# Optimization experiments

Measured on AMD Instinct MI355X. Metric: run time of the kernel, lower is better.

## Reference

```python
import jax, jax.numpy as jnp
import numpy as np

N = 20000      # nodes
E = 200000     # edges
IN = 128       # in_feat
OUT = 128      # out_feat
NB = 8         # num_bases
SI = IN // NB  # submat_in = 16
SO = OUT // NB # submat_out = 16
R = 230        # num_rels
T = 365        # total_times


def setup_inputs() -> dict:
    key = jax.random.key(0)
    ks = jax.random.split(key, 11)
    h = jax.random.normal(ks[0], (N, IN), jnp.float32)
    edge_norm = jax.random.uniform(ks[1], (E, 1), jnp.float32)
    node_norm = jax.random.uniform(ks[2], (N, 1), jnp.float32)
    weight = jax.random.normal(ks[3], (R, NB * SI * SO), jnp.float32) * 0.05
    h_bias = jnp.zeros((OUT,), jnp.float32)
    loop_weight = jax.random.normal(ks[4], (IN, OUT), jnp.float32) * 0.05
    time_embed = jax.random.normal(ks[5], (T, IN), jnp.float32) * 0.05
    edge_src = jax.random.randint(ks[6], (E,), 0, N)
    edge_dst = jax.random.randint(ks[7], (E,), 0, N)
    edge_type = jax.random.randint(ks[8], (E,), 0, R)
    time_idx = jax.random.randint(ks[9], (N,), 0, T)
    return dict(h=h, edge_norm=edge_norm, node_norm=node_norm, weight=weight,
                h_bias=h_bias, loop_weight=loop_weight, time_embed=time_embed,
                edge_src=edge_src, edge_dst=edge_dst, edge_type=edge_type,
                time_idx=time_idx)


def reference(h, edge_norm, node_norm, weight, h_bias, loop_weight, time_embed,
              edge_src, edge_dst, edge_type, time_idx):
    # self-loop message
    loop_message = h @ loop_weight                              # [N, OUT]
    # msg_func: per-edge relation weight gather + block-diagonal bmm
    W_e = weight[edge_type].reshape(-1, NB, SI, SO)             # [E, NB, SI, SO]
    src = h[edge_src].reshape(-1, NB, SI)                       # [E, NB, SI]
    msg = jnp.einsum('ebi,ebio->ebo', src, W_e).reshape(-1, OUT)  # [E, OUT]
    msg = msg * edge_norm
    # fn.sum aggregation over destination nodes
    agg = jax.ops.segment_sum(msg, edge_dst, num_segments=N)    # [N, OUT]
    # apply_func: scale by node norm, then bias + self loop + activation
    node_repr = agg * node_norm
    node_repr = node_repr + h_bias + loop_message
    node_repr = jax.nn.relu(node_repr)
    # get_time_embedding: per-node time embedding gather
    time_embedding = time_embed[time_idx]                       # [N, IN]
    return node_repr, time_embedding
```

## Files before the change

kernel.cpp:

```cpp
#include <hip/hip_runtime.h>
#include <hip/hip_bf16.h>

#define N 20000
#define E 200000
#define IN 128
#define OUT 128
#define NB 8
#define SI 16
#define SO 16
#define R 230
#define T 365

__device__ float g_agg[(size_t)N * OUT];

__global__ void zero_agg_kernel() {
    long i = (long)blockIdx.x * blockDim.x + threadIdx.x;
    long stride = (long)gridDim.x * blockDim.x;
    for (; i < (long)N * OUT; i += stride) g_agg[i] = 0.f;
}

__global__ void edge_kernel(const float* __restrict__ h,
                            const float* __restrict__ edge_norm,
                            const float* __restrict__ weight,
                            const int* __restrict__ edge_src,
                            const int* __restrict__ edge_dst,
                            const int* __restrict__ edge_type) {
    long idx = (long)blockIdx.x * blockDim.x + threadIdx.x;
    int e = (int)(idx >> 7);
    if (e >= E) return;
    int o  = (int)(idx & 127);
    int b  = o >> 4;
    int ol = o & 15;
    int s = edge_src[e];
    int d = edge_dst[e];
    int r = edge_type[e];
    const float* src = h + (long)s * IN + b * SI;
    const float* W   = weight + (long)r * (NB * SI * SO) + b * (SI * SO) + ol;
    float acc = 0.f;
#pragma unroll
    for (int i = 0; i < SI; ++i)
        acc = fmaf(src[i], W[i * SO], acc);
    acc *= edge_norm[e];
    atomicAdd(&g_agg[(long)d * OUT + o], acc);
}

__global__ __launch_bounds__(128) void node_kernel(
        const float* __restrict__ h,
        const float* __restrict__ node_norm,
        const float* __restrict__ h_bias,
        const float* __restrict__ loop_weight,
        const float* __restrict__ time_embed,
        const int* __restrict__ time_idx,
        float* __restrict__ out) {
    __shared__ float hsm[IN * 16];
    const int tid  = threadIdx.x;
    const int base = blockIdx.x * 16;

    for (int k = tid; k < 16 * IN; k += 128) {
        int nl = k >> 7;
        int i  = k & 127;
        hsm[i * 16 + nl] = h[(long)(base + nl) * IN + i];
    }
    __syncthreads();

    float acc[16];
#pragma unroll
    for (int nl = 0; nl < 16; ++nl) acc[nl] = 0.f;

    for (int i = 0; i < IN; ++i) {
        float w = loop_weight[(long)i * OUT + tid];
        const float4* hp = reinterpret_cast<const float4*>(&hsm[i * 16]);
#pragma unroll
        for (int q = 0; q < 4; ++q) {
            float4 hv = hp[q];
            acc[q * 4 + 0] = fmaf(hv.x, w, acc[q * 4 + 0]);
            acc[q * 4 + 1] = fmaf(hv.y, w, acc[q * 4 + 1]);
            acc[q * 4 + 2] = fmaf(hv.z, w, acc[q * 4 + 2]);
            acc[q * 4 + 3] = fmaf(hv.w, w, acc[q * 4 + 3]);
        }
    }

    float bias = h_bias[tid];
#pragma unroll
    for (int nl = 0; nl < 16; ++nl) {
        int n = base + nl;
        float v = g_agg[(long)n * OUT + tid] * node_norm[n] + bias + acc[nl];
        out[(long)n * OUT + tid] = fmaxf(v, 0.f);
        out[(long)N * OUT + (long)n * IN + tid] =
            time_embed[(long)time_idx[n] * IN + tid];
    }
}

extern "C" void kernel_launch(void* const* d_in, const int* in_sizes, int n_in,
                              void* d_out, int out_size, void* d_ws, size_t ws_size,
                              hipStream_t stream) {
    const float* h           = (const float*)d_in[0];
    const float* edge_norm   = (const float*)d_in[1];
    const float* node_norm   = (const float*)d_in[2];
    const float* weight      = (const float*)d_in[3];
    const float* h_bias      = (const float*)d_in[4];
    const float* loop_weight = (const float*)d_in[5];
    const float* time_embed  = (const float*)d_in[6];
    const int*   edge_src    = (const int*)d_in[7];
    const int*   edge_dst    = (const int*)d_in[8];
    const int*   edge_type   = (const int*)d_in[9];
    const int*   time_idx    = (const int*)d_in[10];
    float* out = (float*)d_out;

    zero_agg_kernel<<<2560, 256, 0, stream>>>();

    const long total = (long)E * 128;
    const int  bs = 256;
    edge_kernel<<<(int)((total + bs - 1) / bs), bs, 0, stream>>>(
        h, edge_norm, weight, edge_src, edge_dst, edge_type);

    node_kernel<<<N / 16, 128, 0, stream>>>(
        h, node_norm, h_bias, loop_weight, time_embed, time_idx, out);
}
```

Baseline: 239.9 us.

## Replace atomic scatter with per-destination bf16 message slots and fused aux work

```diff
diff --git a/kernel.cpp b/kernel.cpp
--- a/kernel.cpp
+++ b/kernel.cpp
@@ -1,5 +1,4 @@
 #include <hip/hip_runtime.h>
-#include <hip/hip_bf16.h>
 
 #define N 20000
 #define E 200000
@@ -10,85 +9,206 @@
 #define SO 16
 #define R 230
 #define T 365
-
-__device__ float g_agg[(size_t)N * OUT];
-
-__global__ void zero_agg_kernel() {
-    long i = (long)blockIdx.x * blockDim.x + threadIdx.x;
-    long stride = (long)gridDim.x * blockDim.x;
-    for (; i < (long)N * OUT; i += stride) g_agg[i] = 0.f;
-}
-
-__global__ void edge_kernel(const float* __restrict__ h,
-                            const float* __restrict__ edge_norm,
-                            const float* __restrict__ weight,
-                            const int* __restrict__ edge_src,
-                            const int* __restrict__ edge_dst,
-                            const int* __restrict__ edge_type) {
-    long idx = (long)blockIdx.x * blockDim.x + threadIdx.x;
-    int e = (int)(idx >> 7);
-    if (e >= E) return;
-    int o  = (int)(idx & 127);
-    int b  = o >> 4;
-    int ol = o & 15;
-    int s = edge_src[e];
-    int d = edge_dst[e];
-    int r = edge_type[e];
-    const float* src = h + (long)s * IN + b * SI;
-    const float* W   = weight + (long)r * (NB * SI * SO) + b * (SI * SO) + ol;
-    float acc = 0.f;
-#pragma unroll
-    for (int i = 0; i < SI; ++i)
-        acc = fmaf(src[i], W[i * SO], acc);
-    acc *= edge_norm[e];
-    atomicAdd(&g_agg[(long)d * OUT + o], acc);
-}
-
-__global__ __launch_bounds__(128) void node_kernel(
+#define CAP 64
+
+#define MSG_TILES (E / 32)
+#define SL_BLOCKS 625
+#define TE_BLOCKS 313
+#define AUX_BLOCKS (SL_BLOCKS + TE_BLOCKS)
+#define GRID2 (AUX_BLOCKS * 8)
+
+__device__ float  g_W_t[(size_t)R * NB * SO * SI];
+__device__ ushort g_msg[(size_t)N * CAP * OUT];
+__device__ float  g_sl[(size_t)N * OUT];
+__device__ int    g_cur_d[N];
+
+__device__ __forceinline__ ushort f2bf(float f) {
+    unsigned u = __float_as_uint(f);
+    return (ushort)((u + 0x7fffu + ((u >> 16) & 1u)) >> 16);
+}
+__device__ __forceinline__ float bflo(unsigned m) { return __uint_as_float(m << 16); }
+__device__ __forceinline__ float bfhi(unsigned m) { return __uint_as_float(m & 0xffff0000u); }
+
+__global__ __launch_bounds__(256) void wt_kernel(const float* __restrict__ weight) {
+    int t = blockIdx.x * 256 + threadIdx.x;
+    if (t < R * NB * SI * SO) {
+        int r  = t >> 11;
+        int b  = (t >> 8) & 7;
+        int ol = (t >> 4) & 15;
+        int i  = t & 15;
+        g_W_t[t] = weight[(size_t)r * 2048 + b * 256 + i * 16 + ol];
+    }
+}
+
+__global__ __launch_bounds__(256) void fused_kernel(
         const float* __restrict__ h,
-        const float* __restrict__ node_norm,
+        const float* __restrict__ edge_norm,
+        const int* __restrict__ edge_src,
+        const int* __restrict__ edge_dst,
+        const int* __restrict__ edge_type,
+        const float* __restrict__ loop_weight,
         const float* __restrict__ h_bias,
-        const float* __restrict__ loop_weight,
         const float* __restrict__ time_embed,
         const int* __restrict__ time_idx,
         float* __restrict__ out) {
-    __shared__ float hsm[IN * 16];
-    const int tid  = threadIdx.x;
-    const int base = blockIdx.x * 16;
-
-    for (int k = tid; k < 16 * IN; k += 128) {
-        int nl = k >> 7;
-        int i  = k & 127;
-        hsm[i * 16 + nl] = h[(long)(base + nl) * IN + i];
+    __shared__ __attribute__((aligned(16))) float hsm[32 * 132];
+    __shared__ int   ssrc[32], stype[32], spos[32];
+    __shared__ float snorm[32];
+
+    const int bid = blockIdx.x;
+    const int tid = threadIdx.x;
+
+    if ((bid & 7) == 7) {
+        const int a = bid >> 3;
+        if (a < SL_BLOCKS) {
+            const int q    = tid & 63;
+            const int wave = tid >> 6;
+            const int nb   = a * 32 + wave * 8;
+            const float2* lw2 = reinterpret_cast<const float2*>(loop_weight);
+            float sL[8], sH[8];
+#pragma unroll
+            for (int j = 0; j < 8; ++j) { sL[j] = 0.f; sH[j] = 0.f; }
+            for (int i0 = 0; i0 < IN; i0 += 4) {
+                float2 w0 = lw2[(size_t)(i0 + 0) * 64 + q];
+                float2 w1 = lw2[(size_t)(i0 + 1) * 64 + q];
+                float2 w2 = lw2[(size_t)(i0 + 2) * 64 + q];
+                float2 w3 = lw2[(size_t)(i0 + 3) * 64 + q];
+#pragma unroll
+                for (int j = 0; j < 8; ++j) {
+                    float4 v = *reinterpret_cast<const float4*>(
+                        h + (size_t)(nb + j) * IN + i0);
+                    sL[j] = fmaf(v.x, w0.x, sL[j]); sL[j] = fmaf(v.y, w1.x, sL[j]);
+                    sL[j] = fmaf(v.z, w2.x, sL[j]); sL[j] = fmaf(v.w, w3.x, sL[j]);
+                    sH[j] = fmaf(v.x, w0.y, sH[j]); sH[j] = fmaf(v.y, w1.y, sH[j]);
+                    sH[j] = fmaf(v.z, w2.y, sH[j]); sH[j] = fmaf(v.w, w3.y, sH[j]);
+                }
+            }
+            const float2 bias = reinterpret_cast<const float2*>(h_bias)[q];
+            float2* sl2 = reinterpret_cast<float2*>(g_sl);
+#pragma unroll
+            for (int j = 0; j < 8; ++j) {
+                float2 v; v.x = sL[j] + bias.x; v.y = sH[j] + bias.y;
+                sl2[(size_t)(nb + j) * 64 + q] = v;
+            }
+        } else {
+            const int c    = a - SL_BLOCKS;
+            const int row  = tid >> 2;
+            const int part = tid & 3;
+            const int n    = c * 64 + row;
+            if (n < N) {
+                const float4* src = reinterpret_cast<const float4*>(
+                    time_embed + (size_t)time_idx[n] * IN);
+                float4* dst = reinterpret_cast<float4*>(
+                    out + (size_t)N * OUT + (size_t)n * IN);
+#pragma unroll
+                for (int j = 0; j < 8; ++j)
+                    dst[part * 8 + j] = src[part * 8 + j];
+            }
+        }
+        return;
+    }
+
+    const int t = bid - ((bid + 1) >> 3);
+    if (t >= MSG_TILES) return;
+
+    if (tid < 32) {
+        int e = t * 32 + tid;
+        ssrc[tid]  = edge_src[e];
+        stype[tid] = edge_type[e];
+        snorm[tid] = edge_norm[e];
+        int d = edge_dst[e];
+        int slot = atomicAdd(&g_cur_d[d], 1);
+        if (slot > CAP - 1) slot = CAP - 1;
+        spos[tid] = d * CAP + slot;
     }
     __syncthreads();
 
-    float acc[16];
-#pragma unroll
-    for (int nl = 0; nl < 16; ++nl) acc[nl] = 0.f;
-
-    for (int i = 0; i < IN; ++i) {
-        float w = loop_weight[(long)i * OUT + tid];
-        const float4* hp = reinterpret_cast<const float4*>(&hsm[i * 16]);
-#pragma unroll
-        for (int q = 0; q < 4; ++q) {
-            float4 hv = hp[q];
-            acc[q * 4 + 0] = fmaf(hv.x, w, acc[q * 4 + 0]);
-            acc[q * 4 + 1] = fmaf(hv.y, w, acc[q * 4 + 1]);
-            acc[q * 4 + 2] = fmaf(hv.z, w, acc[q * 4 + 2]);
-            acc[q * 4 + 3] = fmaf(hv.w, w, acc[q * 4 + 3]);
-        }
-    }
-
-    float bias = h_bias[tid];
-#pragma unroll
-    for (int nl = 0; nl < 16; ++nl) {
-        int n = base + nl;
-        float v = g_agg[(long)n * OUT + tid] * node_norm[n] + bias + acc[nl];
-        out[(long)n * OUT + tid] = fmaxf(v, 0.f);
-        out[(long)N * OUT + (long)n * IN + tid] =
-            time_embed[(long)time_idx[n] * IN + tid];
-    }
+    {
+        const int row = tid >> 3;
+        const int c0  = (tid & 7) * 4;
+        const float* hp = h + (size_t)ssrc[row] * IN;
+        float* dst = &hsm[row * 132];
+#pragma unroll
+        for (int j = 0; j < 4; ++j) {
+            float4 v = *reinterpret_cast<const float4*>(hp + c0 + 32 * j);
+            *reinterpret_cast<float4*>(dst + c0 + 32 * j) = v;
+        }
+    }
+    __syncthreads();
+
+    const int slot = tid >> 7;
+    const int o    = tid & 127;
+    const int b    = o >> 4;
+    const int ol   = o & 15;
+
+#pragma unroll 2
+    for (int k = slot; k < 32; k += 2) {
+        const float4* wp = reinterpret_cast<const float4*>(
+            g_W_t + (size_t)stype[k] * 2048 + b * 256 + ol * 16);
+        float4 w0 = wp[0], w1 = wp[1], w2 = wp[2], w3 = wp[3];
+        const float* hrow = &hsm[k * 132 + b * 16];
+        float4 h0 = *reinterpret_cast<const float4*>(hrow);
+        float4 h1 = *reinterpret_cast<const float4*>(hrow + 4);
+        float4 h2 = *reinterpret_cast<const float4*>(hrow + 8);
+        float4 h3 = *reinterpret_cast<const float4*>(hrow + 12);
+        float m0 = 0.f, m1 = 0.f;
+        m0 = fmaf(h0.x, w0.x, m0); m0 = fmaf(h0.y, w0.y, m0);
+        m0 = fmaf(h0.z, w0.z, m0); m0 = fmaf(h0.w, w0.w, m0);
+        m1 = fmaf(h1.x, w1.x, m1); m1 = fmaf(h1.y, w1.y, m1);
+        m1 = fmaf(h1.z, w1.z, m1); m1 = fmaf(h1.w, w1.w, m1);
+        m0 = fmaf(h2.x, w2.x, m0); m0 = fmaf(h2.y, w2.y, m0);
+        m0 = fmaf(h2.z, w2.z, m0); m0 = fmaf(h2.w, w2.w, m0);
+        m1 = fmaf(h3.x, w3.x, m1); m1 = fmaf(h3.y, w3.y, m1);
+        m1 = fmaf(h3.z, w3.z, m1); m1 = fmaf(h3.w, w3.w, m1);
+        __builtin_nontemporal_store(f2bf(snorm[k] * (m0 + m1)),
+                                    &g_msg[(size_t)spos[k] * OUT + o]);
+    }
+}
+
+__global__ __launch_bounds__(256) void node_kernel(
+        const float* __restrict__ node_norm,
+        float* __restrict__ out) {
+    const int t    = threadIdx.x;
+    const int q    = t & 63;
+    const int wave = t >> 6;
+    const int base = blockIdx.x * 8 + wave * 2;
+
+    const unsigned* msg32 = reinterpret_cast<const unsigned*>(g_msg);
+    const float2*   sl2   = reinterpret_cast<const float2*>(g_sl);
+    float2*         o2    = reinterpret_cast<float2*>(out);
+
+#pragma unroll
+    for (int nl = 0; nl < 2; ++nl) {
+        const int n  = base + nl;
+        int cn = g_cur_d[n];
+        if (cn > CAP) cn = CAP;
+        const unsigned* mp = msg32 + (size_t)n * CAP * 64 + q;
+        float aL0 = 0.f, aL1 = 0.f, aH0 = 0.f, aH1 = 0.f;
+        int k = 0;
+        for (; k + 3 < cn; k += 4) {
+            unsigned m0 = __builtin_nontemporal_load(mp + (size_t)(k + 0) * 64);
+            unsigned m1 = __builtin_nontemporal_load(mp + (size_t)(k + 1) * 64);
+            unsigned m2 = __builtin_nontemporal_load(mp + (size_t)(k + 2) * 64);
+            unsigned m3 = __builtin_nontemporal_load(mp + (size_t)(k + 3) * 64);
+            aL0 += bflo(m0); aH0 += bfhi(m0);
+            aL1 += bflo(m1); aH1 += bfhi(m1);
+            aL0 += bflo(m2); aH0 += bfhi(m2);
+            aL1 += bflo(m3); aH1 += bfhi(m3);
+        }
+        for (; k < cn; ++k) {
+            unsigned m = __builtin_nontemporal_load(mp + (size_t)k * 64);
+            aL0 += bflo(m); aH0 += bfhi(m);
+        }
+        const float nn = node_norm[n];
+        const float2 sl = sl2[(size_t)n * 64 + q];
+        float2 v;
+        v.x = fmaxf((aL0 + aL1) * nn + sl.x, 0.f);
+        v.y = fmaxf((aH0 + aH1) * nn + sl.y, 0.f);
+        o2[(size_t)n * 64 + q] = v;
+    }
+
+    __syncthreads();
+    if (t < 8) g_cur_d[blockIdx.x * 8 + t] = 0;
 }
 
 extern "C" void kernel_launch(void* const* d_in, const int* in_sizes, int n_in,
@@ -107,13 +227,9 @@
     const int*   time_idx    = (const int*)d_in[10];
     float* out = (float*)d_out;
 
-    zero_agg_kernel<<<2560, 256, 0, stream>>>();
-
-    const long total = (long)E * 128;
-    const int  bs = 256;
-    edge_kernel<<<(int)((total + bs - 1) / bs), bs, 0, stream>>>(
-        h, edge_norm, weight, edge_src, edge_dst, edge_type);
-
-    node_kernel<<<N / 16, 128, 0, stream>>>(
-        h, node_norm, h_bias, loop_weight, time_embed, time_idx, out);
-}
+    wt_kernel<<<(R * NB * SI * SO + 255) / 256, 256, 0, stream>>>(weight);
+    fused_kernel<<<GRID2, 256, 0, stream>>>(h, edge_norm, edge_src, edge_dst,
+                                            edge_type, loop_weight, h_bias,
+                                            time_embed, time_idx, out);
+    node_kernel<<<N / 8, 256, 0, stream>>>(node_norm, out);
+}
```

New measurement: 344.2 us. +43.4%, slower.
